# Performance work log

Hardware: AMD Instinct MI355X
Metric: run time of the kernel (lower is better)

The kernel has to match this reference:

```python
import jax, jax.numpy as jnp
import numpy as np
import math

NUM_HEADS = 16
KEY_SIZE = 64
HIDDEN = 4096
EMBED = 1024
VOCAB = 32000
SEQ = 2048
LAYERS = 4


def rmsnorm(x):
    return x * jax.lax.rsqrt(jnp.mean(x * x, axis=-1, keepdims=True) + 1e-5)


def rope_buffers(seq, d):
    half = d // 2
    i = jnp.arange(d)
    offset = i % half
    scales = jnp.power(10000.0, (-2.0 / d) * offset.astype(jnp.float32))
    m = jnp.arange(seq, dtype=jnp.float32)
    angles = m[:, None] * scales[None, :]  # [S, D]
    cos = jnp.cos(angles)
    sin = jnp.sin(angles)
    sin = jnp.concatenate([-sin[:, :half], sin[:, half:]], axis=-1)
    return cos, sin


def rotate(x, cos, sin):
    # x: [B, H, S, D]; cos/sin: [S, D]
    half = KEY_SIZE // 2
    swapped = jnp.concatenate([x[..., half:], x[..., :half]], axis=-1)
    return cos[None, None] * x + sin[None, None] * swapped


def setup_inputs() -> dict:
    key = jax.random.key(0)
    ks = jax.random.split(key, 7)
    std = 0.02
    return {
        'tokens': jax.random.randint(ks[0], (1, SEQ), 0, VOCAB),
        'table': jax.random.normal(ks[1], (VOCAB, EMBED), jnp.float32) * std,
        'qkv_w': jax.random.normal(ks[2], (LAYERS, EMBED, 3 * NUM_HEADS * KEY_SIZE), jnp.float32) * std,
        'out_w': jax.random.normal(ks[3], (LAYERS, NUM_HEADS * KEY_SIZE, EMBED), jnp.float32) * std,
        'up_w': jax.random.normal(ks[4], (LAYERS, EMBED, 2 * HIDDEN), jnp.float32) * std,
        'down_w': jax.random.normal(ks[5], (LAYERS, HIDDEN, EMBED), jnp.float32) * std,
        'vocab_w': jax.random.normal(ks[6], (EMBED, VOCAB), jnp.float32) * std,
    }


def reference(tokens, table, qkv_w, out_w, up_w, down_w, vocab_w):
    B, S = tokens.shape
    H, D = NUM_HEADS, KEY_SIZE
    # module zeroes embedding row 0 each forward
    table = table.at[0].set(0.0)
    cos, sin = rope_buffers(S, D)
    causal = jnp.tril(jnp.ones((S, S), dtype=bool))  # context_size == S -> pure causal
    emb = table[tokens]  # [B, S, E]
    for l in range(LAYERS):
        # --- self attention ---
        normed = rmsnorm(emb)
        qkv = normed @ qkv_w[l]  # [B, S, 3HD]
        q, k, v = jnp.split(qkv, 3, axis=-1)
        q = q.reshape(B, S, H, D).transpose(0, 2, 1, 3)
        k = k.reshape(B, S, H, D).transpose(0, 2, 1, 3)
        v = v.reshape(B, S, H, D).transpose(0, 2, 1, 3)
        q = rotate(q, cos, sin)
        k = rotate(k, cos, sin)
        attn = jnp.einsum('bhqd,bhkd->bhqk', q, k) / math.sqrt(D)
        attn = jnp.where(causal[None, None], attn, -jnp.inf)
        attn = jax.nn.softmax(attn, axis=-1)
        out = jnp.einsum('bhqk,bhkd->bhqd', attn, v)
        out = out.transpose(0, 2, 1, 3).reshape(B, S, H * D)
        emb = emb + out @ out_w[l]
        # --- SwiGLU FFN ---
        normed = rmsnorm(emb)
        gate_up = normed @ up_w[l]
        gate, up = gate_up[..., :HIDDEN], gate_up[..., HIDDEN:]
        emb = emb + (up * jax.nn.silu(gate)) @ down_w[l]
    emb = rmsnorm(emb)
    logits = emb @ vocab_w  # [B, S, V]
    return logits
```

## Files before the change

kernel.cpp:

```cpp
#include <hip/hip_runtime.h>
#include <hip/hip_bf16.h>

typedef __attribute__((ext_vector_type(8))) short short8;
typedef __attribute__((ext_vector_type(4))) float f32x4;

__device__ __forceinline__ ushort f2bf(float f) {
  uint32_t u = __float_as_uint(f);
  uint32_t r = (u + 0x7FFFu + ((u >> 16) & 1u)) >> 16;
  return (ushort)r;
}
__device__ __forceinline__ float bf2f(ushort u) {
  return __uint_as_float(((uint32_t)u) << 16);
}

__device__ __forceinline__ void gload_lds16(const ushort* g, ushort* l) {
  __builtin_amdgcn_global_load_lds(
      (const __attribute__((address_space(1))) void*)g,
      (__attribute__((address_space(3))) void*)l, 16, 0, 0);
}

__device__ __forceinline__ f32x4 mfma16(short8 a, short8 b, f32x4 c) {
  return __builtin_amdgcn_mfma_f32_16x16x32_bf16(a, b, c, 0, 0, 0);
}

#define BAR() __builtin_amdgcn_s_barrier()
#define WAIT_LGKM()                                        \
  do {                                                     \
    asm volatile("s_waitcnt lgkmcnt(0)" ::: "memory");     \
    __builtin_amdgcn_sched_barrier(0);                     \
  } while (0)
#define WAIT_VM0()                                         \
  do {                                                     \
    asm volatile("s_waitcnt vmcnt(0)" ::: "memory");       \
    __builtin_amdgcn_sched_barrier(0);                     \
  } while (0)
#define WAIT_VM4()                                         \
  do {                                                     \
    asm volatile("s_waitcnt vmcnt(4)" ::: "memory");       \
    __builtin_amdgcn_sched_barrier(0);                     \
  } while (0)

__global__ __launch_bounds__(256)
void transpose_conv_kernel(const float* __restrict__ W, ushort* __restrict__ WT,
                           const int K, const int N, const int mode) {
  const size_t lofs = (size_t)blockIdx.z * K * N;
  W += lofs;
  WT += lofs;
  __shared__ float tile[64][65];
  const int n0 = blockIdx.x * 64;
  const int k0 = blockIdx.y * 64;
  const int t = threadIdx.x;
#pragma unroll
  for (int j = 0; j < 4; ++j) {
    const int idx = j * 1024 + t * 4;
    const int kk = idx >> 6, nn = idx & 63;
    *(float4*)&tile[kk][nn] = *(const float4*)&W[(size_t)(k0 + kk) * N + n0 + nn];
  }
  __syncthreads();
#pragma unroll
  for (int j = 0; j < 4; ++j) {
    const int idx = j * 1024 + t * 4;
    const int nn = idx >> 6, kk = idx & 63;
    int rr = n0 + nn;
    if (mode == 1) rr = (rr < 4096) ? (2 * rr) : (2 * (rr - 4096) + 1);
    ushort4 o;
    o.x = f2bf(tile[kk + 0][nn]);
    o.y = f2bf(tile[kk + 1][nn]);
    o.z = f2bf(tile[kk + 2][nn]);
    o.w = f2bf(tile[kk + 3][nn]);
    *(ushort4*)&WT[(size_t)rr * K + k0 + kk] = o;
  }
}

__global__ __launch_bounds__(256)
void sincos_kernel(float2* __restrict__ cstab) {
  const int idx = blockIdx.x * 256 + threadIdx.x;
  const int s = idx >> 5, o = idx & 31;
  const float freq = exp2f(-0.41524101186092029f * (float)o);
  const float a = (float)s * freq;
  cstab[idx] = make_float2(cosf(a), sinf(a));
}

__global__ __launch_bounds__(256)
void embed_norm_kernel(const int* __restrict__ tokens, const float* __restrict__ table,
                       float* __restrict__ emb, ushort* __restrict__ normed) {
  const int s = blockIdx.x, t = threadIdx.x;
  const int tok = tokens[s];
  float4 v = make_float4(0.f, 0.f, 0.f, 0.f);
  if (tok != 0) v = *(const float4*)&table[(size_t)tok * 1024 + t * 4];
  *(float4*)&emb[(size_t)s * 1024 + t * 4] = v;
  float ss = v.x * v.x + v.y * v.y + v.z * v.z + v.w * v.w;
#pragma unroll
  for (int off = 32; off; off >>= 1) ss += __shfl_xor(ss, off);
  __shared__ float red[4];
  if ((t & 63) == 0) red[t >> 6] = ss;
  __syncthreads();
  const float total = red[0] + red[1] + red[2] + red[3];
  const float sc = rsqrtf(total * (1.f / 1024.f) + 1e-5f);
  ushort4 o;
  o.x = f2bf(v.x * sc); o.y = f2bf(v.y * sc);
  o.z = f2bf(v.z * sc); o.w = f2bf(v.w * sc);
  *(ushort4*)&normed[(size_t)s * 1024 + t * 4] = o;
}

__global__ __launch_bounds__(256)
void rmsnorm_kernel(const float* __restrict__ x, ushort* __restrict__ out) {
  const int row = blockIdx.x, t = threadIdx.x;
  const float4 v = *(const float4*)&x[(size_t)row * 1024 + t * 4];
  float ss = v.x * v.x + v.y * v.y + v.z * v.z + v.w * v.w;
#pragma unroll
  for (int off = 32; off; off >>= 1) ss += __shfl_xor(ss, off);
  __shared__ float red[4];
  if ((t & 63) == 0) red[t >> 6] = ss;
  __syncthreads();
  const float total = red[0] + red[1] + red[2] + red[3];
  const float sc = rsqrtf(total * (1.f / 1024.f) + 1e-5f);
  ushort4 o;
  o.x = f2bf(v.x * sc); o.y = f2bf(v.y * sc);
  o.z = f2bf(v.z * sc); o.w = f2bf(v.w * sc);
  *(ushort4*)&out[(size_t)row * 1024 + t * 4] = o;
}

__global__ __launch_bounds__(256)
void vtrans_kernel(const ushort* __restrict__ vh, ushort* __restrict__ vt) {
  __shared__ ushort tv[64][68];
  const int h = blockIdx.y;
  const int s0 = blockIdx.x * 64;
  const int t = threadIdx.x;
#pragma unroll
  for (int j = 0; j < 4; ++j) {
    const int idx = j * 1024 + t * 4;
    const int s = idx >> 6, d4 = idx & 63;
    *(ushort4*)&tv[s][d4] = *(const ushort4*)&vh[((size_t)h * 2048 + s0 + s) * 64 + d4];
  }
  __syncthreads();
#pragma unroll
  for (int j = 0; j < 4; ++j) {
    const int idx = j * 1024 + t * 4;
    const int d = idx >> 6, s4 = idx & 63;
    ushort4 ov;
    ov.x = tv[s4 + 0][d];
    ov.y = tv[s4 + 1][d];
    ov.z = tv[s4 + 2][d];
    ov.w = tv[s4 + 3][d];
    *(ushort4*)&vt[((size_t)h * 64 + d) * 2048 + s0 + s4] = ov;
  }
}

__global__ __launch_bounds__(256)
void attn_mfma_kernel(const ushort* __restrict__ qh, const ushort* __restrict__ kh,
                      const ushort* __restrict__ vt, ushort* __restrict__ attn_out) {
  __shared__ ushort sQ[64 * 64];
  __shared__ ushort sK[64 * 64];
  __shared__ ushort sV[64 * 64];
  __shared__ ushort sP[4][1024];
  const int h = blockIdx.y;
  const int bx = blockIdx.x;
  const int qt = (h < 8) ? bx : 31 - bx;
  const int i0 = qt * 64;
  const int tid = threadIdx.x;
  const int w = tid >> 6, lane = tid & 63;
  const int llo = lane & 15, lhi = lane >> 4;
  const int lr = lane >> 3, lc = lane & 7;
  const ushort* qg = qh + ((size_t)h * 2048 + i0) * 64;
  const ushort* kg = kh + (size_t)h * 2048 * 64;
  const ushort* vg = vt + (size_t)h * 64 * 2048;

#pragma unroll
  for (int j = 0; j < 2; ++j) {
    const int r0 = (w * 2 + j) * 8;
    const int row = r0 + lr;
    gload_lds16(qg + (size_t)row * 64 + ((lc ^ (row & 7)) * 8), &sQ[r0 * 64]);
  }
  __syncthreads();
  const int qrow = w * 16 + llo;
  const short8 qf0 = *(const short8*)&sQ[qrow * 64 + ((lhi ^ (qrow & 7)) * 8)];
  const short8 qf1 = *(const short8*)&sQ[qrow * 64 + (((4 + lhi) ^ (qrow & 7)) * 8)];

  float m = -1e30f, lsum = 0.f;
  f32x4 o[4] = {};
  const int nch = qt + 1;
  for (int cb = 0; cb < nch; ++cb) {
    const int kb = cb * 64;
    __syncthreads();
#pragma unroll
    for (int j = 0; j < 2; ++j) {
      const int r0 = (w * 2 + j) * 8;
      const int row = r0 + lr;
      gload_lds16(kg + (size_t)(kb + row) * 64 + ((lc ^ (row & 7)) * 8), &sK[r0 * 64]);
      gload_lds16(vg + (size_t)row * 2048 + kb + ((lc ^ (row & 7)) * 8), &sV[r0 * 64]);
    }
    __syncthreads();

    f32x4 st[4] = {};
#pragma unroll
    for (int ck = 0; ck < 2; ++ck) {
      const short8 qf = ck ? qf1 : qf0;
#pragma unroll
      for (int f = 0; f < 4; ++f) {
        const int key = f * 16 + llo;
        const short8 kf = *(const short8*)&sK[key * 64 + (((ck * 4 + lhi) ^ (key & 7)) * 8)];
        st[f] = mfma16(kf, qf, st[f]);
      }
    }

    float pv[4][4];
    const bool diag = (kb == i0);
#pragma unroll
    for (int f = 0; f < 4; ++f)
#pragma unroll
      for (int r = 0; r < 4; ++r) {
        float x = st[f][r] * 0.125f;
        if (diag && (f * 16 + lhi * 4 + r) > qrow) x = -1e30f;
        pv[f][r] = x;
      }
    float mr = pv[0][0];
#pragma unroll
    for (int f = 0; f < 4; ++f)
#pragma unroll
      for (int r = 0; r < 4; ++r) mr = fmaxf(mr, pv[f][r]);
    mr = fmaxf(mr, __shfl_xor(mr, 16));
    mr = fmaxf(mr, __shfl_xor(mr, 32));
    const float mnew = fmaxf(m, mr);
    const float scale = __expf(m - mnew);
    m = mnew;
    float rs = 0.f;
#pragma unroll
    for (int f = 0; f < 4; ++f)
#pragma unroll
      for (int r = 0; r < 4; ++r) {
        const float p = __expf(pv[f][r] - mnew);
        pv[f][r] = p;
        rs += p;
      }
    rs += __shfl_xor(rs, 16);
    rs += __shfl_xor(rs, 32);
    lsum = lsum * scale + rs;
    float scr[4];
#pragma unroll
    for (int r = 0; r < 4; ++r) scr[r] = __shfl(scale, lhi * 4 + r);
#pragma unroll
    for (int nn = 0; nn < 4; ++nn)
#pragma unroll
      for (int r = 0; r < 4; ++r) o[nn][r] *= scr[r];

    ushort* pw = sP[w];
#pragma unroll
    for (int f = 0; f < 4; ++f) {
      uint2 pk;
      pk.x = (uint)f2bf(pv[f][0]) | ((uint)f2bf(pv[f][1]) << 16);
      pk.y = (uint)f2bf(pv[f][2]) | ((uint)f2bf(pv[f][3]) << 16);
      *(uint2*)&pw[llo * 64 + ((f * 16 + lhi * 4) ^ ((llo & 7) << 3))] = pk;
    }
    const short8 pf0 = *(const short8*)&pw[llo * 64 + ((lhi ^ (llo & 7)) * 8)];
    const short8 pf1 = *(const short8*)&pw[llo * 64 + (((4 + lhi) ^ (llo & 7)) * 8)];

#pragma unroll
    for (int ck = 0; ck < 2; ++ck) {
      const short8 pf = ck ? pf1 : pf0;
#pragma unroll
      for (int nn = 0; nn < 4; ++nn) {
        const int drow = nn * 16 + llo;
        const short8 vf = *(const short8*)&sV[drow * 64 + (((ck * 4 + lhi) ^ (drow & 7)) * 8)];
        o[nn] = mfma16(pf, vf, o[nn]);
      }
    }
  }

  const float inv = 1.f / lsum;
  float invr[4];
#pragma unroll
  for (int r = 0; r < 4; ++r) invr[r] = __shfl(inv, lhi * 4 + r);
#pragma unroll
  for (int nn = 0; nn < 4; ++nn)
#pragma unroll
    for (int r = 0; r < 4; ++r) {
      const int row = i0 + w * 16 + lhi * 4 + r;
      attn_out[(size_t)row * 1024 + h * 64 + nn * 16 + llo] = f2bf(o[nn][r] * invr[r]);
    }
}

template <int BM, int BN, int EPI>
__global__ __launch_bounds__(256)
void gemm_bt_kernel(const ushort* __restrict__ A, const ushort* __restrict__ BT,
                    const float* __restrict__ addend, void* __restrict__ Cout,
                    const int M, const int N, const int K) {
  constexpr int WM = BM / 2, WN = BN / 2;
  constexpr int FM = WM / 16, FN = WN / 16;
  constexpr int CHA = BM / 16, CHB = BN / 16;
  __shared__ ushort sA[BM * 32];
  __shared__ ushort sB[BN * 32];
  const int bm0 = blockIdx.y * BM;
  const int bn0 = blockIdx.x * BN;
  const int tid = threadIdx.x;
  const int wid = tid >> 6;
  const int lane = tid & 63;
  const int wr = wid >> 1, wc = wid & 1;
  const int lhi = lane >> 4, llo = lane & 15;
  f32x4 acc[FM][FN] = {};
  for (int kt = 0; kt < K; kt += 32) {
#pragma unroll
    for (int c2 = 0; c2 < CHA / 4; ++c2) {
      const int ch = c2 * 4 + wid;
      const int e = ch * 512 + lane * 8;
      gload_lds16(A + (size_t)(bm0 + (e >> 5)) * K + kt + (e & 31), sA + ch * 512);
    }
#pragma unroll
    for (int c2 = 0; c2 < CHB / 4; ++c2) {
      const int ch = c2 * 4 + wid;
      const int e = ch * 512 + lane * 8;
      gload_lds16(BT + (size_t)(bn0 + (e >> 5)) * K + kt + (e & 31), sB + ch * 512);
    }
    __syncthreads();
    short8 aF[FM], bF[FN];
#pragma unroll
    for (int mm = 0; mm < FM; ++mm)
      aF[mm] = *(const short8*)&sA[(wr * WM + mm * 16 + llo) * 32 + lhi * 8];
#pragma unroll
    for (int nn = 0; nn < FN; ++nn)
      bF[nn] = *(const short8*)&sB[(wc * WN + nn * 16 + llo) * 32 + lhi * 8];
#pragma unroll
    for (int mm = 0; mm < FM; ++mm)
#pragma unroll
      for (int nn = 0; nn < FN; ++nn)
        acc[mm][nn] = __builtin_amdgcn_mfma_f32_16x16x32_bf16(aF[mm], bF[nn],
                                                              acc[mm][nn], 0, 0, 0);
    __syncthreads();
  }
#pragma unroll
  for (int mm = 0; mm < FM; ++mm) {
#pragma unroll
    for (int nn = 0; nn < FN; ++nn) {
      const int col = bn0 + wc * WN + nn * 16 + llo;
#pragma unroll
      for (int r = 0; r < 4; ++r) {
        const int row = bm0 + wr * WM + mm * 16 + lhi * 4 + r;
        float v = acc[mm][nn][r];
        if constexpr (EPI == 1) v += addend[(size_t)row * N + col];
        ((float*)Cout)[(size_t)row * N + col] = v;
      }
    }
  }
}

__global__ __launch_bounds__(256)
void gemm_qkv_kernel(const ushort* __restrict__ A, const ushort* __restrict__ BT,
                     const float2* __restrict__ cstab, ushort* __restrict__ qh,
                     ushort* __restrict__ kh, ushort* __restrict__ vh, const int K) {
  constexpr int BM = 64, BN = 128, WM = 32, WN = 64, FM = 2, FN = 4;
  constexpr int CHA = BM / 16, CHB = BN / 16;
  __shared__ ushort sA[BM * 32];
  __shared__ ushort sB[BN * 32];
  const int bm0 = blockIdx.y * BM;
  const int bn0 = blockIdx.x * BN;
  const int tid = threadIdx.x;
  const int wid = tid >> 6;
  const int lane = tid & 63;
  const int wr = wid >> 1, wc = wid & 1;
  const int lhi = lane >> 4, llo = lane & 15;
  f32x4 acc[FM][FN] = {};
  for (int kt = 0; kt < K; kt += 32) {
#pragma unroll
    for (int c2 = 0; c2 < CHA / 4; ++c2) {
      const int ch = c2 * 4 + wid;
      const int e = ch * 512 + lane * 8;
      gload_lds16(A + (size_t)(bm0 + (e >> 5)) * K + kt + (e & 31), sA + ch * 512);
    }
#pragma unroll
    for (int c2 = 0; c2 < CHB / 4; ++c2) {
      const int ch = c2 * 4 + wid;
      const int e = ch * 512 + lane * 8;
      gload_lds16(BT + (size_t)(bn0 + (e >> 5)) * K + kt + (e & 31), sB + ch * 512);
    }
    __syncthreads();
    short8 aF[FM], bF[FN];
#pragma unroll
    for (int mm = 0; mm < FM; ++mm)
      aF[mm] = *(const short8*)&sA[(wr * WM + mm * 16 + llo) * 32 + lhi * 8];
#pragma unroll
    for (int nn = 0; nn < FN; ++nn)
      bF[nn] = *(const short8*)&sB[(wc * WN + nn * 16 + llo) * 32 + lhi * 8];
#pragma unroll
    for (int mm = 0; mm < FM; ++mm)
#pragma unroll
      for (int nn = 0; nn < FN; ++nn)
        acc[mm][nn] = mfma16(aF[mm], bF[nn], acc[mm][nn]);
    __syncthreads();
  }
#pragma unroll
  for (int mm = 0; mm < FM; ++mm) {
#pragma unroll
    for (int nn = 0; nn < FN; ++nn) {
      const int col = bn0 + wc * WN + nn * 16 + llo;
      const int part = col >> 10;
      const int hcol = col & 1023;
      const int h = hcol >> 6;
      const int d = hcol & 63;
      const int off = d & 31;
#pragma unroll
      for (int r = 0; r < 4; ++r) {
        const int row = bm0 + wr * WM + mm * 16 + lhi * 4 + r;
        const float v = acc[mm][nn][r];
        const size_t ho = ((size_t)h * 2048 + row) * 64 + d;
        if (part == 2) {
          vh[ho] = f2bf(v);
        } else {
          const float pt = acc[mm][nn ^ 2][r];
          const float2 cn = cstab[row * 32 + off];
          const float si = (d < 32) ? -cn.y : cn.y;
          const ushort o = f2bf(cn.x * v + si * pt);
          if (part == 0) qh[ho] = o; else kh[ho] = o;
        }
      }
    }
  }
}

#define LDA_(MH)                                                              \
  {                                                                           \
    _Pragma("unroll") for (int mm = 0; mm < 4; ++mm) {                        \
      const int row = wr * 128 + ((MH) * 4 + mm) * 16 + llo;                  \
      _Pragma("unroll") for (int ks = 0; ks < 2; ++ks)                        \
          aF[mm][ks] = *(const short8*)&cA[row * 64 +                         \
                          (((ks * 4 + lhi) ^ (row & 7)) * 8)];                \
    }                                                                         \
  }
#define LDB_(NH)                                                              \
  {                                                                           \
    _Pragma("unroll") for (int nn = 0; nn < 2; ++nn) {                        \
      const int row = wc * 64 + ((NH) * 2 + nn) * 16 + llo;                   \
      _Pragma("unroll") for (int ks = 0; ks < 2; ++ks)                        \
          bF[nn][ks] = *(const short8*)&cB[row * 64 +                         \
                          (((ks * 4 + lhi) ^ (row & 7)) * 8)];                \
    }                                                                         \
  }
#define MFMAQ_(MH, NH)                                                        \
  {                                                                           \
    __builtin_amdgcn_s_setprio(1);                                            \
    _Pragma("unroll") for (int mm = 0; mm < 4; ++mm)                          \
        _Pragma("unroll") for (int nn = 0; nn < 2; ++nn)                      \
            _Pragma("unroll") for (int ks = 0; ks < 2; ++ks)                  \
                acc[(MH) * 4 + mm][(NH) * 2 + nn] =                           \
                    mfma16(aF[mm][ks], bF[nn][ks],                            \
                           acc[(MH) * 4 + mm][(NH) * 2 + nn]);                \
    __builtin_amdgcn_s_setprio(0);                                            \
  }

template <int EPI>
__global__ __launch_bounds__(512, 2)
void gemm8_kernel(const ushort* __restrict__ A, const ushort* __restrict__ BT,
                  void* __restrict__ Cout,
                  const int M, const int N, const int K, const int nby) {
  extern __shared__ ushort smem[];
  const int nwg = gridDim.x;
  const int cpx = nwg >> 3;
  int id = blockIdx.x;
  id = (id & 7) * cpx + (id >> 3);
  const int by = id % nby, bx = id / nby;
  const int bm0 = by * 256, bn0 = bx * 256;
  const int tid = threadIdx.x;
  const int wid = tid >> 6, lane = tid & 63;
  const int wr = wid >> 2, wc = wid & 3;
  const int llo = lane & 15, lhi = lane >> 4;
  const ushort* gA = A + (size_t)bm0 * K;
  const ushort* gB = BT + (size_t)bn0 * K;

  auto stage = [&](const ushort* g, ushort* dst, int kt) {
#pragma unroll
    for (int i = 0; i < 4; ++i) {
      const int chunk = i * 512 + wid * 64 + lane;
      const int row = chunk >> 3, c = chunk & 7;
      gload_lds16(g + (size_t)row * K + kt + ((c ^ (row & 7)) * 8),
                  dst + (size_t)(i * 512 + wid * 64) * 8);
    }
  };

  f32x4 acc[8][4] = {};
  short8 aF[4][2];
  short8 bF[2][2];

  stage(gA, smem, 0);
  stage(gB, smem + 16384, 0);
  WAIT_VM0();
  BAR();

  const int nt = K >> 6;
  for (int t = 0; t < nt; ++t) {
    const int cur = t & 1;
    ushort* cA = smem + cur * 32768;
    ushort* cB = cA + 16384;
    ushort* nA = smem + (cur ^ 1) * 32768;
    ushort* nB = nA + 16384;
    const bool pf = (t + 1 < nt);
    LDA_(0); LDB_(0);
    if (pf) { stage(gA, nA, (t + 1) * 64); stage(gB, nB, (t + 1) * 64); }
    BAR(); WAIT_LGKM();
    MFMAQ_(0, 0);
    BAR();
    LDB_(1);
    BAR(); WAIT_LGKM();
    MFMAQ_(0, 1);
    BAR();
    LDA_(1);
    BAR(); WAIT_LGKM();
    MFMAQ_(1, 1);
    BAR();
    LDB_(0);
    BAR(); WAIT_LGKM();
    MFMAQ_(1, 0);
    if (pf) WAIT_VM0();
    BAR();
  }

#pragma unroll
  for (int m = 0; m < 8; ++m) {
#pragma unroll
    for (int n = 0; n < 4; ++n) {
      const int col = bn0 + wc * 64 + n * 16 + llo;
#pragma unroll
      for (int r = 0; r < 4; ++r) {
        const int row = bm0 + wr * 128 + m * 16 + lhi * 4 + r;
        float v = acc[m][n][r];
        if constexpr (EPI == 3) {
          const float other = __shfl_xor(v, 1);
          if ((llo & 1) == 0) {
            const float gate = v, up = other;
            const float hh = up * gate / (1.f + expf(-gate));
            ((ushort*)Cout)[(size_t)row * (N >> 1) + (col >> 1)] = f2bf(hh);
          }
        } else {
          ((float*)Cout)[(size_t)row * N + col] = v;
        }
      }
    }
  }
}

template <int EPI>
__global__ __launch_bounds__(512, 2)
void gemm8p_kernel(const ushort* __restrict__ A, const ushort* __restrict__ BT,
                   void* __restrict__ Cout,
                   const int M, const int N, const int K, const int nby) {
  extern __shared__ ushort smem[];
  const int nwg = gridDim.x;
  const int cpx = nwg >> 3;
  int id = blockIdx.x;
  id = (id & 7) * cpx + (id >> 3);
  const int by = id % nby, bx = id / nby;
  const int bm0 = by * 256, bn0 = bx * 256;
  const int tid = threadIdx.x;
  const int wid = tid >> 6, lane = tid & 63;
  const int wr = wid >> 2, wc = wid & 3;
  const int llo = lane & 15, lhi = lane >> 4;
  const ushort* gA = A + (size_t)bm0 * K;
  const ushort* gB = BT + (size_t)bn0 * K;

  auto stage = [&](ushort* dst, int kt) {
#pragma unroll
    for (int i = 0; i < 2; ++i) {
      const int cb = i * 512 + wid * 64;
      const int ch = cb + lane;
      const int row = ch >> 2, c = ch & 3;
      gload_lds16(gA + (size_t)row * K + kt + ((c ^ ((row >> 1) & 3)) * 8),
                  dst + (size_t)cb * 8);
    }
#pragma unroll
    for (int i = 0; i < 2; ++i) {
      const int cb = i * 512 + wid * 64;
      const int ch = cb + lane;
      const int row = ch >> 2, c = ch & 3;
      gload_lds16(gB + (size_t)row * K + kt + ((c ^ ((row >> 1) & 3)) * 8),
                  dst + 8192 + (size_t)cb * 8);
    }
  };

  f32x4 acc[8][4] = {};
  short8 aF[4], bF[4];

  const int nt = K >> 5;
  stage(smem, 0);
  stage(smem + 16384, 32);
  WAIT_VM4();
  BAR();

  int cs = 0;
  for (int t = 0; t < nt; ++t) {
    ushort* cA = smem + cs * 16384;
    ushort* cB = cA + 8192;
    int ss = cs + 2; if (ss >= 3) ss -= 3;
    const bool pf2 = (t + 2 < nt);
    if (pf2) stage(smem + ss * 16384, (t + 2) * 32);
#pragma unroll
    for (int mm = 0; mm < 4; ++mm) {
      const int row = wr * 128 + mm * 16 + llo;
      aF[mm] = *(const short8*)&cA[row * 32 + ((lhi ^ ((row >> 1) & 3)) * 8)];
    }
#pragma unroll
    for (int nn = 0; nn < 4; ++nn) {
      const int row = wc * 64 + nn * 16 + llo;
      bF[nn] = *(const short8*)&cB[row * 32 + ((lhi ^ ((row >> 1) & 3)) * 8)];
    }
    BAR(); WAIT_LGKM();
    __builtin_amdgcn_s_setprio(1);
#pragma unroll
    for (int mm = 0; mm < 4; ++mm)
#pragma unroll
      for (int nn = 0; nn < 4; ++nn)
        acc[mm][nn] = mfma16(aF[mm], bF[nn], acc[mm][nn]);
    __builtin_amdgcn_s_setprio(0);
    BAR();
#pragma unroll
    for (int mm = 0; mm < 4; ++mm) {
      const int row = wr * 128 + (mm + 4) * 16 + llo;
      aF[mm] = *(const short8*)&cA[row * 32 + ((lhi ^ ((row >> 1) & 3)) * 8)];
    }
    BAR(); WAIT_LGKM();
    __builtin_amdgcn_s_setprio(1);
#pragma unroll
    for (int mm = 0; mm < 4; ++mm)
#pragma unroll
      for (int nn = 0; nn < 4; ++nn)
        acc[mm + 4][nn] = mfma16(aF[mm], bF[nn], acc[mm + 4][nn]);
    __builtin_amdgcn_s_setprio(0);
    if (pf2) { WAIT_VM4(); } else { WAIT_VM0(); }
    BAR();
    ++cs; if (cs == 3) cs = 0;
  }

#pragma unroll
  for (int m = 0; m < 8; ++m) {
#pragma unroll
    for (int n = 0; n < 4; ++n) {
      const int col = bn0 + wc * 64 + n * 16 + llo;
#pragma unroll
      for (int r = 0; r < 4; ++r) {
        const int row = bm0 + wr * 128 + m * 16 + lhi * 4 + r;
        ((float*)Cout)[(size_t)row * N + col] = acc[m][n][r];
      }
    }
  }
}

extern "C" void kernel_launch(void* const* d_in, const int* in_sizes, int n_in,
                              void* d_out, int out_size, void* d_ws, size_t ws_size,
                              hipStream_t stream) {
  const int* tokens    = (const int*)d_in[0];
  const float* table   = (const float*)d_in[1];
  const float* qkv_w   = (const float*)d_in[2];
  const float* out_w   = (const float*)d_in[3];
  const float* up_w    = (const float*)d_in[4];
  const float* down_w  = (const float*)d_in[5];
  const float* vocab_w = (const float*)d_in[6];
  float* logits = (float*)d_out;

  constexpr int G8_LDS = 131072;
  constexpr int G8P_LDS = 98304;
  hipFuncSetAttribute(reinterpret_cast<const void*>(&gemm8_kernel<3>),
                      hipFuncAttributeMaxDynamicSharedMemorySize, G8_LDS);
  hipFuncSetAttribute(reinterpret_cast<const void*>(&gemm8p_kernel<0>),
                      hipFuncAttributeMaxDynamicSharedMemorySize, G8P_LDS);

  char* p = (char*)d_ws;
  auto alloc = [&](size_t bytes) {
    char* r = p;
    p += (bytes + 255) & ~(size_t)255;
    return r;
  };
  float*  emb    = (float*)alloc(2048ull * 1024 * 4);
  ushort* normed = (ushort*)alloc(2048ull * 1024 * 2);
  float2* cstab  = (float2*)alloc(2048ull * 32 * 8);
  ushort* qhb    = (ushort*)alloc(16ull * 2048 * 64 * 2);
  ushort* khb    = (ushort*)alloc(16ull * 2048 * 64 * 2);
  ushort* vhb    = (ushort*)alloc(16ull * 2048 * 64 * 2);
  ushort* vtb    = (ushort*)alloc(16ull * 64 * 2048 * 2);
  ushort* attno  = (ushort*)alloc(2048ull * 1024 * 2);
  ushort* hbuf   = (ushort*)alloc(2048ull * 4096 * 2);
  ushort* qkvT   = (ushort*)alloc(4ull * 3072 * 1024 * 2);
  ushort* outT   = (ushort*)alloc(4ull * 1024 * 1024 * 2);
  ushort* upT    = (ushort*)alloc(4ull * 8192 * 1024 * 2);
  ushort* downT  = (ushort*)alloc(4ull * 1024 * 4096 * 2);
  ushort* vocabT = (ushort*)alloc(32000ull * 1024 * 2);

  transpose_conv_kernel<<<dim3(3072 / 64, 1024 / 64, 4), 256, 0, stream>>>(
      qkv_w, qkvT, 1024, 3072, 0);
  transpose_conv_kernel<<<dim3(1024 / 64, 1024 / 64, 4), 256, 0, stream>>>(
      out_w, outT, 1024, 1024, 0);
  transpose_conv_kernel<<<dim3(8192 / 64, 1024 / 64, 4), 256, 0, stream>>>(
      up_w, upT, 1024, 8192, 1);
  transpose_conv_kernel<<<dim3(1024 / 64, 4096 / 64, 4), 256, 0, stream>>>(
      down_w, downT, 4096, 1024, 0);
  transpose_conv_kernel<<<dim3(32000 / 64, 1024 / 64, 1), 256, 0, stream>>>(
      vocab_w, vocabT, 1024, 32000, 0);
  sincos_kernel<<<256, 256, 0, stream>>>(cstab);

  embed_norm_kernel<<<2048, 256, 0, stream>>>(tokens, table, emb, normed);

  for (int l = 0; l < 4; ++l) {
    if (l > 0) rmsnorm_kernel<<<2048, 256, 0, stream>>>(emb, normed);
    gemm_qkv_kernel<<<dim3(3072 / 128, 2048 / 64), 256, 0, stream>>>(
        normed, qkvT + (size_t)l * 3072 * 1024, cstab, qhb, khb, vhb, 1024);
    vtrans_kernel<<<dim3(32, 16), 256, 0, stream>>>(vhb, vtb);
    attn_mfma_kernel<<<dim3(32, 16), 256, 0, stream>>>(qhb, khb, vtb, attno);
    gemm_bt_kernel<64, 128, 1><<<dim3(1024 / 128, 2048 / 64), 256, 0, stream>>>(
        attno, outT + (size_t)l * 1024 * 1024, emb, emb, 2048, 1024, 1024);
    rmsnorm_kernel<<<2048, 256, 0, stream>>>(emb, normed);
    gemm8_kernel<3><<<(8192 / 256) * (2048 / 256), 512, G8_LDS, stream>>>(
        normed, upT + (size_t)l * 8192 * 1024, hbuf, 2048, 8192, 1024, 2048 / 256);
    gemm_bt_kernel<64, 128, 1><<<dim3(1024 / 128, 2048 / 64), 256, 0, stream>>>(
        hbuf, downT + (size_t)l * 1024 * 4096, emb, emb, 2048, 1024, 4096);
  }
  rmsnorm_kernel<<<2048, 256, 0, stream>>>(emb, normed);
  gemm8p_kernel<0><<<(32000 / 256) * (2048 / 256), 512, G8P_LDS, stream>>>(
      normed, vocabT, logits, 2048, 32000, 1024, 2048 / 256);
}
```

Baseline: 1.317 ms.

## Use K=64 swizzled LDS tiles in small GEMMs and fuse V transpose into QKV

The out-proj, down-proj and QKV GEMMs now stage 64-wide K tiles with an XOR-swizzled LDS layout, which halves the number of barriers per K and avoids LDS bank conflicts. The QKV GEMM grows to 128x128 tiles. Its epilogue writes V directly in transposed layout, which removes the separate vtrans kernel and the vh buffer. The larger tiles use more LDS and registers, and the QKV grid shrinks to 384 blocks, so occupancy and parallelism may drop.

Result: faster. 1.241 ms (-5.8%).

```diff
diff --git a/kernel.cpp b/kernel.cpp
--- a/kernel.cpp
+++ b/kernel.cpp
@@ -119,32 +119,6 @@
   o.x = f2bf(v.x * sc); o.y = f2bf(v.y * sc);
   o.z = f2bf(v.z * sc); o.w = f2bf(v.w * sc);
   *(ushort4*)&out[(size_t)row * 1024 + t * 4] = o;
-}
-
-__global__ __launch_bounds__(256)
-void vtrans_kernel(const ushort* __restrict__ vh, ushort* __restrict__ vt) {
-  __shared__ ushort tv[64][68];
-  const int h = blockIdx.y;
-  const int s0 = blockIdx.x * 64;
-  const int t = threadIdx.x;
-#pragma unroll
-  for (int j = 0; j < 4; ++j) {
-    const int idx = j * 1024 + t * 4;
-    const int s = idx >> 6, d4 = idx & 63;
-    *(ushort4*)&tv[s][d4] = *(const ushort4*)&vh[((size_t)h * 2048 + s0 + s) * 64 + d4];
-  }
-  __syncthreads();
-#pragma unroll
-  for (int j = 0; j < 4; ++j) {
-    const int idx = j * 1024 + t * 4;
-    const int d = idx >> 6, s4 = idx & 63;
-    ushort4 ov;
-    ov.x = tv[s4 + 0][d];
-    ov.y = tv[s4 + 1][d];
-    ov.z = tv[s4 + 2][d];
-    ov.w = tv[s4 + 3][d];
-    *(ushort4*)&vt[((size_t)h * 64 + d) * 2048 + s0 + s4] = ov;
-  }
 }
 
 __global__ __launch_bounds__(256)
@@ -282,49 +256,60 @@
 
 template <int BM, int BN, int EPI>
 __global__ __launch_bounds__(256)
-void gemm_bt_kernel(const ushort* __restrict__ A, const ushort* __restrict__ BT,
-                    const float* __restrict__ addend, void* __restrict__ Cout,
-                    const int M, const int N, const int K) {
+void gemm_bt64_kernel(const ushort* __restrict__ A, const ushort* __restrict__ BT,
+                      const float* __restrict__ addend, void* __restrict__ Cout,
+                      const int M, const int N, const int K) {
   constexpr int WM = BM / 2, WN = BN / 2;
   constexpr int FM = WM / 16, FN = WN / 16;
-  constexpr int CHA = BM / 16, CHB = BN / 16;
-  __shared__ ushort sA[BM * 32];
-  __shared__ ushort sB[BN * 32];
+  __shared__ ushort sA[BM * 64];
+  __shared__ ushort sB[BN * 64];
   const int bm0 = blockIdx.y * BM;
   const int bn0 = blockIdx.x * BN;
   const int tid = threadIdx.x;
-  const int wid = tid >> 6;
-  const int lane = tid & 63;
+  const int wid = tid >> 6, lane = tid & 63;
   const int wr = wid >> 1, wc = wid & 1;
   const int lhi = lane >> 4, llo = lane & 15;
   f32x4 acc[FM][FN] = {};
-  for (int kt = 0; kt < K; kt += 32) {
-#pragma unroll
-    for (int c2 = 0; c2 < CHA / 4; ++c2) {
-      const int ch = c2 * 4 + wid;
-      const int e = ch * 512 + lane * 8;
-      gload_lds16(A + (size_t)(bm0 + (e >> 5)) * K + kt + (e & 31), sA + ch * 512);
-    }
-#pragma unroll
-    for (int c2 = 0; c2 < CHB / 4; ++c2) {
-      const int ch = c2 * 4 + wid;
-      const int e = ch * 512 + lane * 8;
-      gload_lds16(BT + (size_t)(bn0 + (e >> 5)) * K + kt + (e & 31), sB + ch * 512);
+  for (int kt = 0; kt < K; kt += 64) {
+#pragma unroll
+    for (int i = 0; i < BM * 8 / 256; ++i) {
+      const int cb = i * 256 + wid * 64;
+      const int ch = cb + lane;
+      const int row = ch >> 3, c = ch & 7;
+      gload_lds16(A + (size_t)(bm0 + row) * K + kt + ((c ^ (row & 7)) * 8),
+                  sA + (size_t)cb * 8);
+    }
+#pragma unroll
+    for (int i = 0; i < BN * 8 / 256; ++i) {
+      const int cb = i * 256 + wid * 64;
+      const int ch = cb + lane;
+      const int row = ch >> 3, c = ch & 7;
+      gload_lds16(BT + (size_t)(bn0 + row) * K + kt + ((c ^ (row & 7)) * 8),
+                  sB + (size_t)cb * 8);
     }
     __syncthreads();
-    short8 aF[FM], bF[FN];
+    short8 aF[FM][2], bF[FN][2];
+#pragma unroll
+    for (int mm = 0; mm < FM; ++mm) {
+      const int row = wr * WM + mm * 16 + llo;
+#pragma unroll
+      for (int ks = 0; ks < 2; ++ks)
+        aF[mm][ks] = *(const short8*)&sA[row * 64 + (((ks * 4 + lhi) ^ (row & 7)) * 8)];
+    }
+#pragma unroll
+    for (int nn = 0; nn < FN; ++nn) {
+      const int row = wc * WN + nn * 16 + llo;
+#pragma unroll
+      for (int ks = 0; ks < 2; ++ks)
+        bF[nn][ks] = *(const short8*)&sB[row * 64 + (((ks * 4 + lhi) ^ (row & 7)) * 8)];
+    }
 #pragma unroll
     for (int mm = 0; mm < FM; ++mm)
-      aF[mm] = *(const short8*)&sA[(wr * WM + mm * 16 + llo) * 32 + lhi * 8];
-#pragma unroll
-    for (int nn = 0; nn < FN; ++nn)
-      bF[nn] = *(const short8*)&sB[(wc * WN + nn * 16 + llo) * 32 + lhi * 8];
-#pragma unroll
-    for (int mm = 0; mm < FM; ++mm)
 #pragma unroll
       for (int nn = 0; nn < FN; ++nn)
-        acc[mm][nn] = __builtin_amdgcn_mfma_f32_16x16x32_bf16(aF[mm], bF[nn],
-                                                              acc[mm][nn], 0, 0, 0);
+#pragma unroll
+        for (int ks = 0; ks < 2; ++ks)
+          acc[mm][nn] = mfma16(aF[mm][ks], bF[nn][ks], acc[mm][nn]);
     __syncthreads();
   }
 #pragma unroll
@@ -346,49 +331,62 @@
 __global__ __launch_bounds__(256)
 void gemm_qkv_kernel(const ushort* __restrict__ A, const ushort* __restrict__ BT,
                      const float2* __restrict__ cstab, ushort* __restrict__ qh,
-                     ushort* __restrict__ kh, ushort* __restrict__ vh, const int K) {
-  constexpr int BM = 64, BN = 128, WM = 32, WN = 64, FM = 2, FN = 4;
-  constexpr int CHA = BM / 16, CHB = BN / 16;
-  __shared__ ushort sA[BM * 32];
-  __shared__ ushort sB[BN * 32];
+                     ushort* __restrict__ kh, ushort* __restrict__ vt, const int K) {
+  constexpr int BM = 128, BN = 128, WM = 64, WN = 64, FM = 4, FN = 4;
+  __shared__ ushort sA[BM * 64];
+  __shared__ ushort sB[BN * 64];
   const int bm0 = blockIdx.y * BM;
   const int bn0 = blockIdx.x * BN;
   const int tid = threadIdx.x;
-  const int wid = tid >> 6;
-  const int lane = tid & 63;
+  const int wid = tid >> 6, lane = tid & 63;
   const int wr = wid >> 1, wc = wid & 1;
   const int lhi = lane >> 4, llo = lane & 15;
   f32x4 acc[FM][FN] = {};
-  for (int kt = 0; kt < K; kt += 32) {
-#pragma unroll
-    for (int c2 = 0; c2 < CHA / 4; ++c2) {
-      const int ch = c2 * 4 + wid;
-      const int e = ch * 512 + lane * 8;
-      gload_lds16(A + (size_t)(bm0 + (e >> 5)) * K + kt + (e & 31), sA + ch * 512);
-    }
-#pragma unroll
-    for (int c2 = 0; c2 < CHB / 4; ++c2) {
-      const int ch = c2 * 4 + wid;
-      const int e = ch * 512 + lane * 8;
-      gload_lds16(BT + (size_t)(bn0 + (e >> 5)) * K + kt + (e & 31), sB + ch * 512);
+  for (int kt = 0; kt < K; kt += 64) {
+#pragma unroll
+    for (int i = 0; i < 4; ++i) {
+      const int cb = i * 256 + wid * 64;
+      const int ch = cb + lane;
+      const int row = ch >> 3, c = ch & 7;
+      gload_lds16(A + (size_t)(bm0 + row) * K + kt + ((c ^ (row & 7)) * 8),
+                  sA + (size_t)cb * 8);
+    }
+#pragma unroll
+    for (int i = 0; i < 4; ++i) {
+      const int cb = i * 256 + wid * 64;
+      const int ch = cb + lane;
+      const int row = ch >> 3, c = ch & 7;
+      gload_lds16(BT + (size_t)(bn0 + row) * K + kt + ((c ^ (row & 7)) * 8),
+                  sB + (size_t)cb * 8);
     }
     __syncthreads();
-    short8 aF[FM], bF[FN];
+    short8 aF[FM][2], bF[FN][2];
+#pragma unroll
+    for (int mm = 0; mm < FM; ++mm) {
+      const int row = wr * WM + mm * 16 + llo;
+#pragma unroll
+      for (int ks = 0; ks < 2; ++ks)
+        aF[mm][ks] = *(const short8*)&sA[row * 64 + (((ks * 4 + lhi) ^ (row & 7)) * 8)];
+    }
+#pragma unroll
+    for (int nn = 0; nn < FN; ++nn) {
+      const int row = wc * WN + nn * 16 + llo;
+#pragma unroll
+      for (int ks = 0; ks < 2; ++ks)
+        bF[nn][ks] = *(const short8*)&sB[row * 64 + (((ks * 4 + lhi) ^ (row & 7)) * 8)];
+    }
 #pragma unroll
     for (int mm = 0; mm < FM; ++mm)
-      aF[mm] = *(const short8*)&sA[(wr * WM + mm * 16 + llo) * 32 + lhi * 8];
-#pragma unroll
-    for (int nn = 0; nn < FN; ++nn)
-      bF[nn] = *(const short8*)&sB[(wc * WN + nn * 16 + llo) * 32 + lhi * 8];
-#pragma unroll
-    for (int mm = 0; mm < FM; ++mm)
 #pragma unroll
       for (int nn = 0; nn < FN; ++nn)
-        acc[mm][nn] = mfma16(aF[mm], bF[nn], acc[mm][nn]);
+#pragma unroll
+        for (int ks = 0; ks < 2; ++ks)
+          acc[mm][nn] = mfma16(aF[mm][ks], bF[nn][ks], acc[mm][nn]);
     __syncthreads();
   }
 #pragma unroll
   for (int mm = 0; mm < FM; ++mm) {
+    const int row_base = bm0 + wr * WM + mm * 16 + lhi * 4;
 #pragma unroll
     for (int nn = 0; nn < FN; ++nn) {
       const int col = bn0 + wc * WN + nn * 16 + llo;
@@ -397,18 +395,23 @@
       const int h = hcol >> 6;
       const int d = hcol & 63;
       const int off = d & 31;
-#pragma unroll
-      for (int r = 0; r < 4; ++r) {
-        const int row = bm0 + wr * WM + mm * 16 + lhi * 4 + r;
-        const float v = acc[mm][nn][r];
-        const size_t ho = ((size_t)h * 2048 + row) * 64 + d;
-        if (part == 2) {
-          vh[ho] = f2bf(v);
-        } else {
+      if (part == 2) {
+        ushort4 o;
+        o.x = f2bf(acc[mm][nn][0]);
+        o.y = f2bf(acc[mm][nn][1]);
+        o.z = f2bf(acc[mm][nn][2]);
+        o.w = f2bf(acc[mm][nn][3]);
+        *(ushort4*)&vt[((size_t)h * 64 + d) * 2048 + row_base] = o;
+      } else {
+#pragma unroll
+        for (int r = 0; r < 4; ++r) {
+          const int row = row_base + r;
+          const float v = acc[mm][nn][r];
           const float pt = acc[mm][nn ^ 2][r];
           const float2 cn = cstab[row * 32 + off];
           const float si = (d < 32) ? -cn.y : cn.y;
           const ushort o = f2bf(cn.x * v + si * pt);
+          const size_t ho = ((size_t)h * 2048 + row) * 64 + d;
           if (part == 0) qh[ho] = o; else kh[ho] = o;
         }
       }
@@ -671,7 +674,6 @@
   float2* cstab  = (float2*)alloc(2048ull * 32 * 8);
   ushort* qhb    = (ushort*)alloc(16ull * 2048 * 64 * 2);
   ushort* khb    = (ushort*)alloc(16ull * 2048 * 64 * 2);
-  ushort* vhb    = (ushort*)alloc(16ull * 2048 * 64 * 2);
   ushort* vtb    = (ushort*)alloc(16ull * 64 * 2048 * 2);
   ushort* attno  = (ushort*)alloc(2048ull * 1024 * 2);
   ushort* hbuf   = (ushort*)alloc(2048ull * 4096 * 2);
@@ -697,16 +699,15 @@
 
   for (int l = 0; l < 4; ++l) {
     if (l > 0) rmsnorm_kernel<<<2048, 256, 0, stream>>>(emb, normed);
-    gemm_qkv_kernel<<<dim3(3072 / 128, 2048 / 64), 256, 0, stream>>>(
-        normed, qkvT + (size_t)l * 3072 * 1024, cstab, qhb, khb, vhb, 1024);
-    vtrans_kernel<<<dim3(32, 16), 256, 0, stream>>>(vhb, vtb);
+    gemm_qkv_kernel<<<dim3(3072 / 128, 2048 / 128), 256, 0, stream>>>(
+        normed, qkvT + (size_t)l * 3072 * 1024, cstab, qhb, khb, vtb, 1024);
     attn_mfma_kernel<<<dim3(32, 16), 256, 0, stream>>>(qhb, khb, vtb, attno);
-    gemm_bt_kernel<64, 128, 1><<<dim3(1024 / 128, 2048 / 64), 256, 0, stream>>>(
+    gemm_bt64_kernel<64, 128, 1><<<dim3(1024 / 128, 2048 / 64), 256, 0, stream>>>(
         attno, outT + (size_t)l * 1024 * 1024, emb, emb, 2048, 1024, 1024);
     rmsnorm_kernel<<<2048, 256, 0, stream>>>(emb, normed);
     gemm8_kernel<3><<<(8192 / 256) * (2048 / 256), 512, G8_LDS, stream>>>(
         normed, upT + (size_t)l * 8192 * 1024, hbuf, 2048, 8192, 1024, 2048 / 256);
-    gemm_bt_kernel<64, 128, 1><<<dim3(1024 / 128, 2048 / 64), 256, 0, stream>>>(
+    gemm_bt64_kernel<64, 128, 1><<<dim3(1024 / 128, 2048 / 64), 256, 0, stream>>>(
         hbuf, downT + (size_t)l * 1024 * 4096, emb, emb, 2048, 1024, 4096);
   }
   rmsnorm_kernel<<<2048, 256, 0, stream>>>(emb, normed);
```
